# Optimization experiments

Measured on AMD Instinct MI355X. Metric: run time of the kernel, lower is better.

## Reference

```python
import jax, jax.numpy as jnp
import numpy as np

B, N, D, L = 64, 4096, 3, 128  # batch, points, dim, num projections (Markov chain length)
P = 2.0  # p in the loss; degree in projected distance is also 2


def setup_inputs() -> dict:
    key = jax.random.key(0)
    k1, k2 = jax.random.split(key)
    x = jax.random.normal(k1, (B, N, D), dtype=jnp.float32)
    y = jax.random.normal(k2, (B, N, D), dtype=jnp.float32)
    return {"x": x, "y": y}


def _normalize(v):
    return v / jnp.sqrt(jnp.sum(v * v, axis=-1, keepdims=True))


def _proj_dist_multi(x, y, theta):
    # x, y: [B, N, D]; theta: [B, L, D] -> [B, L]
    xp = jnp.einsum('bnd,bld->bln', x, theta)
    yp = jnp.einsum('bnd,bld->bln', y, theta)
    diff = jnp.sort(xp, axis=-1) - jnp.sort(yp, axis=-1)
    return jnp.sum(diff * diff, axis=-1)  # degree = 2


def _proj_dist_single(x, y, theta):
    # theta: [B, D] -> [B]
    xp = jnp.einsum('bnd,bd->bn', x, theta)
    yp = jnp.einsum('bnd,bd->bn', y, theta)
    diff = jnp.sort(xp, axis=-1) - jnp.sort(yp, axis=-1)
    return jnp.sum(diff * diff, axis=-1)


def reference(x, y):
    key = jax.random.key(42)
    theta0 = _normalize(jax.random.normal(jax.random.fold_in(key, 0), (B, D), dtype=x.dtype))
    dist0 = _proj_dist_single(x, y, theta0)

    # IMH chain (torch version runs it under no_grad; we stop_gradient the samples)
    def step(carry, l):
        theta_old, dist_old = carry
        kk = jax.random.fold_in(key, l + 1)
        ka, kb = jax.random.split(kk)
        theta_new = _normalize(jax.random.normal(ka, (B, D), dtype=x.dtype))
        dist_new = _proj_dist_single(x, y, theta_new)
        log_ratio = dist_new - dist_old  # f_type == 'exp'
        acc_rate = jnp.minimum(0.0, log_ratio)
        accept = jnp.log(jax.random.uniform(kb, (B,), dtype=x.dtype)) <= acc_rate
        theta = jnp.where(accept[:, None], theta_new, theta_old)
        dist = jnp.where(accept, dist_new, dist_old)
        return (theta, dist), theta

    (_, _), thetas = jax.lax.scan(step, (theta0, dist0), jnp.arange(L - 1))
    theta = jnp.concatenate([theta0[:, None, :], jnp.swapaxes(thetas, 0, 1)], axis=1)  # [B, L, D]
    theta = jax.lax.stop_gradient(theta)

    distances = _proj_dist_multi(x, y, theta)  # [B, L]
    loss = jnp.mean(jnp.mean(distances, axis=1) ** (1.0 / P))  # gradient_type == 'independent'
    return loss
```

## Files before the change

kernel.cpp:

```cpp
#include <hip/hip_runtime.h>
#include <stdint.h>

#define NB 64
#define NP 4096
#define ND 3
#define NL 128
#define BT 256
#define NR 16

typedef uint32_t u32;
typedef _Float16 half2v __attribute__((ext_vector_type(2)));

__device__ __forceinline__ uint32_t rotl32(uint32_t v, int r) {
  return (v << r) | (v >> (32 - r));
}

__device__ __forceinline__ void threefry2x32(uint32_t k0, uint32_t k1,
                                             uint32_t c0, uint32_t c1,
                                             uint32_t& o0, uint32_t& o1) {
  uint32_t ks2 = k0 ^ k1 ^ 0x1BD11BDAu;
  uint32_t x0 = c0 + k0;
  uint32_t x1 = c1 + k1;
#define TF_RND(R) { x0 += x1; x1 = rotl32(x1, (R)); x1 ^= x0; }
  TF_RND(13) TF_RND(15) TF_RND(26) TF_RND(6)
  x0 += k1;  x1 += ks2 + 1u;
  TF_RND(17) TF_RND(29) TF_RND(16) TF_RND(24)
  x0 += ks2; x1 += k0 + 2u;
  TF_RND(13) TF_RND(15) TF_RND(26) TF_RND(6)
  x0 += k0;  x1 += k1 + 3u;
  TF_RND(17) TF_RND(29) TF_RND(16) TF_RND(24)
  x0 += k1;  x1 += ks2 + 4u;
  TF_RND(13) TF_RND(15) TF_RND(26) TF_RND(6)
  x0 += ks2; x1 += k0 + 5u;
#undef TF_RND
  o0 = x0; o1 = x1;
}

__device__ __forceinline__ float erfinv_f(float x) {
  float w = -log1pf(-x * x);
  float p;
  if (w < 5.0f) {
    w = w - 2.5f;
    p = 2.81022636e-08f;
    p = fmaf(p, w, 3.43273939e-07f);
    p = fmaf(p, w, -3.5233877e-06f);
    p = fmaf(p, w, -4.39150654e-06f);
    p = fmaf(p, w, 0.00021858087f);
    p = fmaf(p, w, -0.00125372503f);
    p = fmaf(p, w, -0.00417768164f);
    p = fmaf(p, w, 0.246640727f);
    p = fmaf(p, w, 1.50140941f);
  } else {
    w = sqrtf(w) - 3.0f;
    p = -0.000200214257f;
    p = fmaf(p, w, 0.000100950558f);
    p = fmaf(p, w, 0.00134934322f);
    p = fmaf(p, w, -0.00367342844f);
    p = fmaf(p, w, 0.00573950773f);
    p = fmaf(p, w, -0.0076224613f);
    p = fmaf(p, w, 0.00943887047f);
    p = fmaf(p, w, 1.00167406f);
    p = fmaf(p, w, 2.83297682f);
  }
  return p * x;
}

__device__ __forceinline__ float bits_to_normal(uint32_t bits) {
  float f = __uint_as_float((bits >> 9) | 0x3F800000u) - 1.0f;
  const float LO = -0.99999994f;
  float u = fmaf(f, 2.0f, LO);
  u = fmaxf(LO, u);
  return 1.41421354f * erfinv_f(u);
}

__device__ __forceinline__ float bits_to_unif01(uint32_t bits) {
  float f = __uint_as_float((bits >> 9) | 0x3F800000u) - 1.0f;
  return fmaxf(0.0f, f);
}

__global__ __launch_bounds__(128) void rng_kernel(float* __restrict__ theta,
                                                  float* __restrict__ logu) {
  const int l = blockIdx.x;
  const int tid = threadIdx.x;

  uint32_t kl0, kl1;
  threefry2x32(0u, 42u, 0u, (uint32_t)l, kl0, kl1);

  uint32_t na0 = kl0, na1 = kl1;
  uint32_t nb0 = 0u, nb1 = 0u;
  if (l > 0) {
    uint32_t a0, b0, a1, b1;
    threefry2x32(kl0, kl1, 0u, 2u, a0, b0);
    threefry2x32(kl0, kl1, 1u, 3u, a1, b1);
    na0 = a0; na1 = a1;
    nb0 = b0; nb1 = b1;
  }

  __shared__ float vals[NB * ND];
  if (tid < 96) {
    uint32_t o0, o1;
    threefry2x32(na0, na1, (uint32_t)tid, (uint32_t)(96 + tid), o0, o1);
    vals[tid] = bits_to_normal(o0);
    vals[96 + tid] = bits_to_normal(o1);
  }
  __syncthreads();

  if (tid < NB) {
    float v0 = vals[tid * 3 + 0];
    float v1 = vals[tid * 3 + 1];
    float v2 = vals[tid * 3 + 2];
    float s = sqrtf(v0 * v0 + v1 * v1 + v2 * v2);
    float* tp = theta + ((size_t)l * NB + tid) * 3;
    tp[0] = v0 / s;
    tp[1] = v1 / s;
    tp[2] = v2 / s;
  }

  if (l > 0 && tid < 32) {
    uint32_t o0, o1;
    threefry2x32(nb0, nb1, (uint32_t)tid, (uint32_t)(32 + tid), o0, o1);
    logu[l * NB + tid] = logf(bits_to_unif01(o0));
    logu[l * NB + 32 + tid] = logf(bits_to_unif01(o1));
  }
}

__device__ __forceinline__ u32 pkmin(u32 a, u32 b) {
  u32 d; asm("v_pk_min_f16 %0, %1, %2" : "=v"(d) : "v"(a), "v"(b)); return d;
}
__device__ __forceinline__ u32 pkmax(u32 a, u32 b) {
  u32 d; asm("v_pk_max_f16 %0, %1, %2" : "=v"(d) : "v"(a), "v"(b)); return d;
}

__device__ __forceinline__ void ceA(u32& a, u32& b) {
  u32 mn = pkmin(a, b), mx = pkmax(a, b); a = mn; b = mx;
}
__device__ __forceinline__ void ceD(u32& a, u32& b) {
  u32 mn = pkmin(a, b), mx = pkmax(a, b); a = mx; b = mn;
}

__device__ __forceinline__ void flipx(u32 (&r)[NR], u32 mask) {
#pragma unroll
  for (int w = 0; w < NR; ++w) r[w] ^= mask;
}
__device__ __forceinline__ u32 fmask(u32 d) {
  return (d << 31) | (d << 15);
}

__device__ __forceinline__ void tailA(u32 (&r)[NR]) {
#pragma unroll
  for (int v = 0; v < 8; ++v) ceA(r[v], r[v + 8]);
#pragma unroll
  for (int v = 0; v < NR; ++v) if (!(v & 4)) ceA(r[v], r[v | 4]);
#pragma unroll
  for (int v = 0; v < NR; ++v) if (!(v & 2)) ceA(r[v], r[v | 2]);
#pragma unroll
  for (int v = 0; v < NR; ++v) if (!(v & 1)) ceA(r[v], r[v | 1]);
}

__device__ __forceinline__ void sort_k2_8(u32 (&r)[NR]) {
  ceA(r[0], r[1]);  ceD(r[2], r[3]);  ceA(r[4], r[5]);  ceD(r[6], r[7]);
  ceA(r[8], r[9]);  ceD(r[10], r[11]); ceA(r[12], r[13]); ceD(r[14], r[15]);
  ceA(r[0], r[2]);  ceA(r[1], r[3]);  ceD(r[4], r[6]);  ceD(r[5], r[7]);
  ceA(r[8], r[10]); ceA(r[9], r[11]); ceD(r[12], r[14]); ceD(r[13], r[15]);
  ceA(r[0], r[1]);  ceA(r[2], r[3]);  ceD(r[4], r[5]);  ceD(r[6], r[7]);
  ceA(r[8], r[9]);  ceA(r[10], r[11]); ceD(r[12], r[13]); ceD(r[14], r[15]);
  ceA(r[0], r[4]);  ceA(r[1], r[5]);  ceA(r[2], r[6]);  ceA(r[3], r[7]);
  ceD(r[8], r[12]); ceD(r[9], r[13]); ceD(r[10], r[14]); ceD(r[11], r[15]);
  ceA(r[0], r[2]);  ceA(r[1], r[3]);  ceA(r[4], r[6]);  ceA(r[5], r[7]);
  ceD(r[8], r[10]); ceD(r[9], r[11]); ceD(r[12], r[14]); ceD(r[13], r[15]);
  ceA(r[0], r[1]);  ceA(r[2], r[3]);  ceA(r[4], r[5]);  ceA(r[6], r[7]);
  ceD(r[8], r[9]);  ceD(r[10], r[11]); ceD(r[12], r[13]); ceD(r[14], r[15]);
}

__device__ __forceinline__ void ce_keep(u32& a, u32 p, bool km) {
  u32 mn = pkmin(a, p), mx = pkmax(a, p);
  a = km ? mn : mx;
}

__device__ __forceinline__ void stage_bperm(u32 (&r)[NR], int addr, bool km) {
  u32 p0, p1, p2, p3, p4, p5, p6, p7, p8, p9, p10, p11, p12, p13, p14, p15;
  asm("ds_bpermute_b32 %0, %16, %17\n\t"
      "ds_bpermute_b32 %1, %16, %18\n\t"
      "ds_bpermute_b32 %2, %16, %19\n\t"
      "ds_bpermute_b32 %3, %16, %20\n\t"
      "ds_bpermute_b32 %4, %16, %21\n\t"
      "ds_bpermute_b32 %5, %16, %22\n\t"
      "ds_bpermute_b32 %6, %16, %23\n\t"
      "ds_bpermute_b32 %7, %16, %24\n\t"
      "ds_bpermute_b32 %8, %16, %25\n\t"
      "ds_bpermute_b32 %9, %16, %26\n\t"
      "ds_bpermute_b32 %10, %16, %27\n\t"
      "ds_bpermute_b32 %11, %16, %28\n\t"
      "ds_bpermute_b32 %12, %16, %29\n\t"
      "ds_bpermute_b32 %13, %16, %30\n\t"
      "ds_bpermute_b32 %14, %16, %31\n\t"
      "ds_bpermute_b32 %15, %16, %32\n\t"
      "s_waitcnt lgkmcnt(0)"
      : "=&v"(p0), "=&v"(p1), "=&v"(p2), "=&v"(p3),
        "=&v"(p4), "=&v"(p5), "=&v"(p6), "=&v"(p7),
        "=&v"(p8), "=&v"(p9), "=&v"(p10), "=&v"(p11),
        "=&v"(p12), "=&v"(p13), "=&v"(p14), "=&v"(p15)
      : "v"(addr),
        "v"(r[0]), "v"(r[1]), "v"(r[2]), "v"(r[3]),
        "v"(r[4]), "v"(r[5]), "v"(r[6]), "v"(r[7]),
        "v"(r[8]), "v"(r[9]), "v"(r[10]), "v"(r[11]),
        "v"(r[12]), "v"(r[13]), "v"(r[14]), "v"(r[15]));
  ce_keep(r[0], p0, km);   ce_keep(r[1], p1, km);
  ce_keep(r[2], p2, km);   ce_keep(r[3], p3, km);
  ce_keep(r[4], p4, km);   ce_keep(r[5], p5, km);
  ce_keep(r[6], p6, km);   ce_keep(r[7], p7, km);
  ce_keep(r[8], p8, km);   ce_keep(r[9], p9, km);
  ce_keep(r[10], p10, km); ce_keep(r[11], p11, km);
  ce_keep(r[12], p12, km); ce_keep(r[13], p13, km);
  ce_keep(r[14], p14, km); ce_keep(r[15], p15, km);
}

template<int MB>
__device__ __forceinline__ void phase_sh(u32 (&r)[NR], int lanesh2, int tid) {
  if constexpr (MB >= 32) stage_bperm(r, lanesh2 ^ 128, (tid & 32) == 0);
  if constexpr (MB >= 16) stage_bperm(r, lanesh2 ^ 64, (tid & 16) == 0);
  if constexpr (MB >= 8) stage_bperm(r, lanesh2 ^ 32, (tid & 8) == 0);
  if constexpr (MB >= 4) stage_bperm(r, lanesh2 ^ 16, (tid & 4) == 0);
  if constexpr (MB >= 2) stage_bperm(r, lanesh2 ^ 8, (tid & 2) == 0);
  if constexpr (MB >= 1) stage_bperm(r, lanesh2 ^ 4, (tid & 1) == 0);
  tailA(r);
}

__global__ __launch_bounds__(BT) void dist_kernel(const float* __restrict__ x,
                                                  const float* __restrict__ y,
                                                  const float* __restrict__ theta,
                                                  float* __restrict__ dist) {
  __shared__ u32 buf[NP];

  const int bid = blockIdx.x;
  const int l = bid & (NL - 1);
  const int b = bid >> 7;
  const int tid = threadIdx.x;

  const float* tp = theta + ((size_t)l * NB + b) * 3;
  const float t0 = tp[0];
  const float t1 = tp[1];
  const float t2 = tp[2];

  u32 r[NR];
  {
    const float4* px = (const float4*)(x + (size_t)b * NP * ND + (size_t)tid * 48);
    const float4* py = (const float4*)(y + (size_t)b * NP * ND + (size_t)tid * 48);
#pragma unroll
    for (int g = 0; g < 4; ++g) {
      float4 XA = px[3 * g], XB = px[3 * g + 1], XC = px[3 * g + 2];
      float4 YA = py[3 * g], YB = py[3 * g + 1], YC = py[3 * g + 2];
      float x0 = XA.x * t0 + XA.y * t1 + XA.z * t2;
      float x1 = XA.w * t0 + XB.x * t1 + XB.y * t2;
      float x2 = XB.z * t0 + XB.w * t1 + XC.x * t2;
      float x3 = XC.y * t0 + XC.z * t1 + XC.w * t2;
      float y0 = YA.x * t0 + YA.y * t1 + YA.z * t2;
      float y1 = YA.w * t0 + YB.x * t1 + YB.y * t2;
      float y2 = YB.z * t0 + YB.w * t1 + YC.x * t2;
      float y3 = YC.y * t0 + YC.z * t1 + YC.w * t2;
      r[4 * g + 0] = __builtin_bit_cast(u32, __builtin_amdgcn_cvt_pkrtz(x0, y0));
      r[4 * g + 1] = __builtin_bit_cast(u32, __builtin_amdgcn_cvt_pkrtz(x1, y1));
      r[4 * g + 2] = __builtin_bit_cast(u32, __builtin_amdgcn_cvt_pkrtz(x2, y2));
      r[4 * g + 3] = __builtin_bit_cast(u32, __builtin_amdgcn_cvt_pkrtz(x3, y3));
    }
  }

  sort_k2_8(r);
  const int lanesh2 = (tid & 63) << 2;

  flipx(r, fmask((u32)tid & 1u));
  tailA(r);
  flipx(r, fmask(((u32)(tid >> 0) ^ (u32)(tid >> 1)) & 1u)); phase_sh<1>(r, lanesh2, tid);
  flipx(r, fmask(((u32)(tid >> 1) ^ (u32)(tid >> 2)) & 1u)); phase_sh<2>(r, lanesh2, tid);
  flipx(r, fmask(((u32)(tid >> 2) ^ (u32)(tid >> 3)) & 1u)); phase_sh<4>(r, lanesh2, tid);
  flipx(r, fmask(((u32)(tid >> 3) ^ (u32)(tid >> 4)) & 1u)); phase_sh<8>(r, lanesh2, tid);
  flipx(r, fmask(((u32)(tid >> 4) ^ (u32)(tid >> 5)) & 1u)); phase_sh<16>(r, lanesh2, tid);
  flipx(r, fmask(((u32)(tid >> 5) ^ (u32)(tid >> 6)) & 1u)); phase_sh<32>(r, lanesh2, tid);

  flipx(r, fmask(((u32)(tid >> 6) ^ (u32)(tid >> 7)) & 1u));
  __syncthreads();
#pragma unroll
  for (int w = 0; w < NR; ++w) buf[w * BT + tid] = r[w];
  __syncthreads();
  {
    const bool km = (tid & 64) == 0;
#pragma unroll
    for (int w = 0; w < NR; ++w) {
      u32 p = buf[w * BT + (tid ^ 64)];
      u32 mn = pkmin(r[w], p), mx = pkmax(r[w], p);
      r[w] = km ? mn : mx;
    }
  }
  phase_sh<32>(r, lanesh2, tid);

  flipx(r, fmask((u32)(tid >> 7) & 1u));
  __syncthreads();
#pragma unroll
  for (int w = 0; w < NR; ++w) buf[w * BT + tid] = r[w];
  __syncthreads();
  {
    const bool a128 = (tid & 128) == 0;
    const bool a64 = (tid & 64) == 0;
#pragma unroll
    for (int w = 0; w < NR; ++w) {
      u32 av = r[w];
      u32 bv = buf[w * BT + (tid ^ 128)];
      u32 cv = buf[w * BT + (tid ^ 64)];
      u32 dv = buf[w * BT + (tid ^ 192)];
      u32 a1 = a128 ? pkmin(av, bv) : pkmax(av, bv);
      u32 c1 = a128 ? pkmin(cv, dv) : pkmax(cv, dv);
      r[w] = a64 ? pkmin(a1, c1) : pkmax(a1, c1);
    }
  }
  phase_sh<32>(r, lanesh2, tid);

  float s = 0.0f;
#pragma unroll
  for (int w = 0; w < NR; ++w) {
    half2v h = __builtin_bit_cast(half2v, r[w]);
    float d = (float)h[0] - (float)h[1];
    s = fmaf(d, d, s);
  }
  for (int off = 32; off; off >>= 1) s += __shfl_down(s, off, 64);
  __syncthreads();
  float* red = (float*)buf;
  if ((tid & 63) == 0) red[tid >> 6] = s;
  __syncthreads();
  if (tid == 0) dist[l * NB + b] = red[0] + red[1] + red[2] + red[3];
}

__global__ __launch_bounds__(64) void chain_kernel(const float* __restrict__ dist,
                                                   const float* __restrict__ logu,
                                                   float* __restrict__ out) {
  const int b = threadIdx.x;
  float dold = dist[b];
  float sum = dold;
  for (int l = 1; l < NL; ++l) {
    float dn = dist[l * NB + b];
    float acc = fminf(0.0f, dn - dold);
    if (logu[l * NB + b] <= acc) dold = dn;
    sum += dold;
  }
  float v = sqrtf(sum * (1.0f / (float)NL));
  for (int off = 32; off; off >>= 1) v += __shfl_down(v, off, 64);
  if (b == 0) out[0] = v * (1.0f / (float)NB);
}

extern "C" void kernel_launch(void* const* d_in, const int* in_sizes, int n_in,
                              void* d_out, int out_size, void* d_ws, size_t ws_size,
                              hipStream_t stream) {
  const float* x = (const float*)d_in[0];
  const float* y = (const float*)d_in[1];
  float* out = (float*)d_out;

  float* theta = (float*)d_ws;
  float* logu = theta + NL * NB * 3;
  float* dist = logu + NL * NB;

  hipLaunchKernelGGL(rng_kernel, dim3(NL), dim3(128), 0, stream, theta, logu);
  hipLaunchKernelGGL(dist_kernel, dim3(NB * NL), dim3(BT), 0, stream, x, y, theta, dist);
  hipLaunchKernelGGL(chain_kernel, dim3(1), dim3(64), 0, stream, dist, logu, out);
}
```

Before: 269.6 us.

## Sort each projection in a single wavefront with 64 registers per lane

Restructures the dist kernel so one 64-lane wavefront sorts all 4096 packed fp16 x/y projections, holding 64 values per lane in registers instead of 16 per thread across 256 threads. This removes the LDS round-trips and __syncthreads barriers for the cross-wave bitonic stages. The two smallest lane-distance exchanges now use DPP moves instead of ds_bpermute. In exchange each thread does four times the in-register compare-exchange work and carries far more VGPRs, which lowers occupancy and may cause spills. The outer phase loops are left un-unrolled, which adds loop overhead.

Result: faster. 254.1 us (-5.8%).

```diff
diff --git a/kernel.cpp b/kernel.cpp
--- a/kernel.cpp
+++ b/kernel.cpp
@@ -5,8 +5,7 @@
 #define NP 4096
 #define ND 3
 #define NL 128
-#define BT 256
-#define NR 16
+#define NE 64
 
 typedef uint32_t u32;
 typedef _Float16 half2v __attribute__((ext_vector_type(2)));
@@ -138,38 +137,21 @@
   u32 mn = pkmin(a, b), mx = pkmax(a, b); a = mx; b = mn;
 }
 
-__device__ __forceinline__ void flipx(u32 (&r)[NR], u32 mask) {
-#pragma unroll
-  for (int w = 0; w < NR; ++w) r[w] ^= mask;
-}
 __device__ __forceinline__ u32 fmask(u32 d) {
   return (d << 31) | (d << 15);
 }
 
-__device__ __forceinline__ void tailA(u32 (&r)[NR]) {
-#pragma unroll
-  for (int v = 0; v < 8; ++v) ceA(r[v], r[v + 8]);
-#pragma unroll
-  for (int v = 0; v < NR; ++v) if (!(v & 4)) ceA(r[v], r[v | 4]);
-#pragma unroll
-  for (int v = 0; v < NR; ++v) if (!(v & 2)) ceA(r[v], r[v | 2]);
-#pragma unroll
-  for (int v = 0; v < NR; ++v) if (!(v & 1)) ceA(r[v], r[v | 1]);
-}
-
-__device__ __forceinline__ void sort_k2_8(u32 (&r)[NR]) {
-  ceA(r[0], r[1]);  ceD(r[2], r[3]);  ceA(r[4], r[5]);  ceD(r[6], r[7]);
-  ceA(r[8], r[9]);  ceD(r[10], r[11]); ceA(r[12], r[13]); ceD(r[14], r[15]);
-  ceA(r[0], r[2]);  ceA(r[1], r[3]);  ceD(r[4], r[6]);  ceD(r[5], r[7]);
-  ceA(r[8], r[10]); ceA(r[9], r[11]); ceD(r[12], r[14]); ceD(r[13], r[15]);
-  ceA(r[0], r[1]);  ceA(r[2], r[3]);  ceD(r[4], r[5]);  ceD(r[6], r[7]);
-  ceA(r[8], r[9]);  ceA(r[10], r[11]); ceD(r[12], r[13]); ceD(r[14], r[15]);
-  ceA(r[0], r[4]);  ceA(r[1], r[5]);  ceA(r[2], r[6]);  ceA(r[3], r[7]);
-  ceD(r[8], r[12]); ceD(r[9], r[13]); ceD(r[10], r[14]); ceD(r[11], r[15]);
-  ceA(r[0], r[2]);  ceA(r[1], r[3]);  ceA(r[4], r[6]);  ceA(r[5], r[7]);
-  ceD(r[8], r[10]); ceD(r[9], r[11]); ceD(r[12], r[14]); ceD(r[13], r[15]);
-  ceA(r[0], r[1]);  ceA(r[2], r[3]);  ceA(r[4], r[5]);  ceA(r[6], r[7]);
-  ceD(r[8], r[9]);  ceD(r[10], r[11]); ceD(r[12], r[13]); ceD(r[14], r[15]);
+__device__ __forceinline__ void flip64(u32 (&r)[NE], u32 mask) {
+#pragma unroll
+  for (int w = 0; w < NE; ++w) r[w] ^= mask;
+}
+
+__device__ __forceinline__ void tail64(u32 (&r)[NE]) {
+#pragma unroll
+  for (int j = 32; j >= 1; j >>= 1)
+#pragma unroll
+    for (int v = 0; v < NE; ++v)
+      if (!(v & j)) ceA(r[v], r[v | j]);
 }
 
 __device__ __forceinline__ void ce_keep(u32& a, u32 p, bool km) {
@@ -177,7 +159,7 @@
   a = km ? mn : mx;
 }
 
-__device__ __forceinline__ void stage_bperm(u32 (&r)[NR], int addr, bool km) {
+__device__ __forceinline__ void stage_bperm16(u32 (&r)[16], int addr, bool km) {
   u32 p0, p1, p2, p3, p4, p5, p6, p7, p8, p9, p10, p11, p12, p13, p14, p15;
   asm("ds_bpermute_b32 %0, %16, %17\n\t"
       "ds_bpermute_b32 %1, %16, %18\n\t"
@@ -215,39 +197,43 @@
   ce_keep(r[14], p14, km); ce_keep(r[15], p15, km);
 }
 
-template<int MB>
-__device__ __forceinline__ void phase_sh(u32 (&r)[NR], int lanesh2, int tid) {
-  if constexpr (MB >= 32) stage_bperm(r, lanesh2 ^ 128, (tid & 32) == 0);
-  if constexpr (MB >= 16) stage_bperm(r, lanesh2 ^ 64, (tid & 16) == 0);
-  if constexpr (MB >= 8) stage_bperm(r, lanesh2 ^ 32, (tid & 8) == 0);
-  if constexpr (MB >= 4) stage_bperm(r, lanesh2 ^ 16, (tid & 4) == 0);
-  if constexpr (MB >= 2) stage_bperm(r, lanesh2 ^ 8, (tid & 2) == 0);
-  if constexpr (MB >= 1) stage_bperm(r, lanesh2 ^ 4, (tid & 1) == 0);
-  tailA(r);
-}
-
-__global__ __launch_bounds__(BT) void dist_kernel(const float* __restrict__ x,
+__device__ __forceinline__ void stage_bperm64(u32 (&r)[NE], int addr, bool km) {
+  stage_bperm16(*reinterpret_cast<u32(*)[16]>(&r[0]), addr, km);
+  stage_bperm16(*reinterpret_cast<u32(*)[16]>(&r[16]), addr, km);
+  stage_bperm16(*reinterpret_cast<u32(*)[16]>(&r[32]), addr, km);
+  stage_bperm16(*reinterpret_cast<u32(*)[16]>(&r[48]), addr, km);
+}
+
+template<int CTRL>
+__device__ __forceinline__ void stage_dpp(u32 (&r)[NE], bool km) {
+#pragma unroll
+  for (int v = 0; v < NE; ++v) {
+    u32 p = (u32)__builtin_amdgcn_update_dpp(0, (int)r[v], CTRL, 0xF, 0xF, true);
+    u32 mn = pkmin(r[v], p), mx = pkmax(r[v], p);
+    r[v] = km ? mn : mx;
+  }
+}
+
+__global__ __launch_bounds__(64) void dist_kernel(const float* __restrict__ x,
                                                   const float* __restrict__ y,
                                                   const float* __restrict__ theta,
                                                   float* __restrict__ dist) {
-  __shared__ u32 buf[NP];
-
   const int bid = blockIdx.x;
   const int l = bid & (NL - 1);
   const int b = bid >> 7;
-  const int tid = threadIdx.x;
+  const int lane = threadIdx.x;
 
   const float* tp = theta + ((size_t)l * NB + b) * 3;
   const float t0 = tp[0];
   const float t1 = tp[1];
   const float t2 = tp[2];
 
-  u32 r[NR];
+  u32 r[NE];
   {
-    const float4* px = (const float4*)(x + (size_t)b * NP * ND + (size_t)tid * 48);
-    const float4* py = (const float4*)(y + (size_t)b * NP * ND + (size_t)tid * 48);
-#pragma unroll
-    for (int g = 0; g < 4; ++g) {
+    const float4* px = (const float4*)(x + (size_t)b * NP * ND + (size_t)lane * 192);
+    const float4* py = (const float4*)(y + (size_t)b * NP * ND + (size_t)lane * 192);
+#pragma unroll
+    for (int g = 0; g < 16; ++g) {
       float4 XA = px[3 * g], XB = px[3 * g + 1], XC = px[3 * g + 2];
       float4 YA = py[3 * g], YB = py[3 * g + 1], YC = py[3 * g + 2];
       float x0 = XA.x * t0 + XA.y * t1 + XA.z * t2;
@@ -265,68 +251,42 @@
     }
   }
 
-  sort_k2_8(r);
-  const int lanesh2 = (tid & 63) << 2;
-
-  flipx(r, fmask((u32)tid & 1u));
-  tailA(r);
-  flipx(r, fmask(((u32)(tid >> 0) ^ (u32)(tid >> 1)) & 1u)); phase_sh<1>(r, lanesh2, tid);
-  flipx(r, fmask(((u32)(tid >> 1) ^ (u32)(tid >> 2)) & 1u)); phase_sh<2>(r, lanesh2, tid);
-  flipx(r, fmask(((u32)(tid >> 2) ^ (u32)(tid >> 3)) & 1u)); phase_sh<4>(r, lanesh2, tid);
-  flipx(r, fmask(((u32)(tid >> 3) ^ (u32)(tid >> 4)) & 1u)); phase_sh<8>(r, lanesh2, tid);
-  flipx(r, fmask(((u32)(tid >> 4) ^ (u32)(tid >> 5)) & 1u)); phase_sh<16>(r, lanesh2, tid);
-  flipx(r, fmask(((u32)(tid >> 5) ^ (u32)(tid >> 6)) & 1u)); phase_sh<32>(r, lanesh2, tid);
-
-  flipx(r, fmask(((u32)(tid >> 6) ^ (u32)(tid >> 7)) & 1u));
-  __syncthreads();
-#pragma unroll
-  for (int w = 0; w < NR; ++w) buf[w * BT + tid] = r[w];
-  __syncthreads();
-  {
-    const bool km = (tid & 64) == 0;
-#pragma unroll
-    for (int w = 0; w < NR; ++w) {
-      u32 p = buf[w * BT + (tid ^ 64)];
-      u32 mn = pkmin(r[w], p), mx = pkmax(r[w], p);
-      r[w] = km ? mn : mx;
-    }
-  }
-  phase_sh<32>(r, lanesh2, tid);
-
-  flipx(r, fmask((u32)(tid >> 7) & 1u));
-  __syncthreads();
-#pragma unroll
-  for (int w = 0; w < NR; ++w) buf[w * BT + tid] = r[w];
-  __syncthreads();
-  {
-    const bool a128 = (tid & 128) == 0;
-    const bool a64 = (tid & 64) == 0;
-#pragma unroll
-    for (int w = 0; w < NR; ++w) {
-      u32 av = r[w];
-      u32 bv = buf[w * BT + (tid ^ 128)];
-      u32 cv = buf[w * BT + (tid ^ 64)];
-      u32 dv = buf[w * BT + (tid ^ 192)];
-      u32 a1 = a128 ? pkmin(av, bv) : pkmax(av, bv);
-      u32 c1 = a128 ? pkmin(cv, dv) : pkmax(cv, dv);
-      r[w] = a64 ? pkmin(a1, c1) : pkmax(a1, c1);
-    }
-  }
-  phase_sh<32>(r, lanesh2, tid);
+#pragma unroll
+  for (int k = 2; k <= 32; k <<= 1)
+#pragma unroll
+    for (int j = k >> 1; j >= 1; j >>= 1)
+#pragma unroll
+      for (int v = 0; v < NE; ++v)
+        if (!(v & j)) {
+          if (!(v & k)) ceA(r[v], r[v | j]);
+          else          ceD(r[v], r[v | j]);
+        }
+
+  flip64(r, fmask((u32)lane & 1u));
+  tail64(r);
+
+  const int lanesh2 = lane << 2;
+#pragma unroll 1
+  for (int p = 0; p < 6; ++p) {
+    flip64(r, fmask(((u32)(lane >> p) ^ (u32)(lane >> (p + 1))) & 1u));
+#pragma unroll 1
+    for (int m = 1 << p; m >= 4; m >>= 1)
+      stage_bperm64(r, lanesh2 ^ (m << 2), (lane & m) == 0);
+    if (p >= 1) stage_dpp<0x4E>(r, (lane & 2) == 0);
+    stage_dpp<0xB1>(r, (lane & 1) == 0);
+    tail64(r);
+  }
 
   float s = 0.0f;
 #pragma unroll
-  for (int w = 0; w < NR; ++w) {
+  for (int w = 0; w < NE; ++w) {
     half2v h = __builtin_bit_cast(half2v, r[w]);
     float d = (float)h[0] - (float)h[1];
     s = fmaf(d, d, s);
   }
+#pragma unroll
   for (int off = 32; off; off >>= 1) s += __shfl_down(s, off, 64);
-  __syncthreads();
-  float* red = (float*)buf;
-  if ((tid & 63) == 0) red[tid >> 6] = s;
-  __syncthreads();
-  if (tid == 0) dist[l * NB + b] = red[0] + red[1] + red[2] + red[3];
+  if (lane == 0) dist[l * NB + b] = s;
 }
 
 __global__ __launch_bounds__(64) void chain_kernel(const float* __restrict__ dist,
@@ -358,6 +318,6 @@
   float* dist = logu + NL * NB;
 
   hipLaunchKernelGGL(rng_kernel, dim3(NL), dim3(128), 0, stream, theta, logu);
-  hipLaunchKernelGGL(dist_kernel, dim3(NB * NL), dim3(BT), 0, stream, x, y, theta, dist);
+  hipLaunchKernelGGL(dist_kernel, dim3(NB * NL), dim3(64), 0, stream, x, y, theta, dist);
   hipLaunchKernelGGL(chain_kernel, dim3(1), dim3(64), 0, stream, dist, logu, out);
 }
```
